# Kernel tuning notes

Hardware: AMD Instinct MI355X
Metric: run time of the kernel (lower is better)

Reference implementation:

```python
import jax, jax.numpy as jnp
import numpy as np


def setup_inputs() -> dict:
    key = jax.random.key(0)
    k1, k2, k3, k4 = jax.random.split(key, 4)
    b, h, w = 16, 28, 28
    C = 3072  # 1024 + 2048
    L1 = 9    # num_landmarks + 1
    K = 2000  # num_classes
    l3 = jax.random.normal(k1, (b, 1024, h, w), dtype=jnp.float32)
    l4 = jax.random.normal(k2, (b, 2048, h // 2, w // 2), dtype=jnp.float32)
    W_land = jax.random.normal(k3, (L1, C), dtype=jnp.float32) * 0.02  # 1x1 conv weight
    W_class = jax.random.normal(k4, (K, C), dtype=jnp.float32) * 0.02
    modulation = jnp.ones((1, C, L1), dtype=jnp.float32)
    return {"l3": l3, "l4": l4, "W_land": W_land, "W_class": W_class, "modulation": modulation}


def reference(l3, l4, W_land, W_class, modulation):
    b, c3, h, w = l3.shape
    # bilinear upsample layer4 to layer3 spatial size (align_corners=False semantics)
    l4_up = jax.image.resize(l4, (l4.shape[0], l4.shape[1], h, w), method="bilinear")
    x = jnp.concatenate([l4_up, l3], axis=1)  # (b, 3072, h, w)

    ab = jnp.einsum("lc,bchw->blhw", W_land, x)            # (b, L+1, h, w)
    b_sq = jnp.sum(x * x, axis=1, keepdims=True)           # (b, 1, h, w)
    a_sq = jnp.sum(W_land * W_land, axis=1)[None, :, None, None]  # (1, L+1, 1, 1)
    maps = jax.nn.softmax(-(b_sq - 2.0 * ab + a_sq), axis=1)      # channel softmax (Softmax2d)

    # weighted spatial pooling: mean over h and w of maps[:,None]*x[:,:,None]
    hw = h * w
    all_features = jnp.einsum("blhw,bchw->bcl", maps, x) / hw     # (b, C, L+1)

    # modulation; dropout layers are identity at inference
    modulated = all_features * modulation                           # (b, C, L+1)
    scores = jnp.einsum("kc,bcl->bkl", W_class, modulated)          # (b, K, L+1)
    class_scores = jnp.mean(scores[:, :, :-1], axis=-1)             # (b, K)
    return class_scores, maps, all_features
```

## Files before the change

### kernel.cpp

```cpp
#include <hip/hip_runtime.h>
#include <math.h>

#define C_TOTAL 3072
#define C4 2048
#define C3 1024
#define HW  784
#define W_  28
#define HW4 196
#define W4  14
#define L_TOT 9
#define NB  16
#define NK  2000
#define CH4 32
#define CH3 32
#define N3SUM (NB * L_TOT * HW)
#define N4SUM (NB * L_TOT * HW4)

__device__ __forceinline__ void up_taps(int o, int& i0, int& i1, float& w0, float& w1) {
    int j = o >> 1;
    if (o & 1) { i0 = j;                       i1 = (j + 1 < W4) ? j + 1 : W4 - 1; w0 = 0.75f; w1 = 0.25f; }
    else       { i0 = (j - 1 > 0) ? j - 1 : 0; i1 = j;                             w0 = 0.25f; w1 = 0.75f; }
}

__device__ __forceinline__ float wdown(int o, int s) {
    int i0, i1; float w0, w1;
    up_taps(o, i0, i1, w0, w1);
    return (i0 == s ? w0 : 0.f) + (i1 == s ? w1 : 0.f);
}

__global__ __launch_bounds__(256) void abx_kernel(
    const float* __restrict__ l3, const float* __restrict__ l4,
    const float* __restrict__ Wl,
    float* __restrict__ ab4p, float* __restrict__ ab3p, float* __restrict__ asqp)
{
    __shared__ float4 red[4][L_TOT][49];

    const int bx = blockIdx.x;
    const int b  = blockIdx.y;
    const int tid = threadIdx.x;

    if (bx < CH4) {
        const int s = tid >> 6;
        const int g = tid & 63;
        const int c0 = bx * 64;
        float4 acc[L_TOT];
        #pragma unroll
        for (int l = 0; l < L_TOT; ++l) acc[l] = make_float4(0.f, 0.f, 0.f, 0.f);
        if (g < 49) {
            const float4* slab = (const float4*)(l4 + ((size_t)b * C4 + c0) * HW4);
            #pragma unroll 8
            for (int i = 0; i < 16; ++i) {
                const int c = s * 16 + i;
                float4 xv = slab[c * 49 + g];
                const float* wc = Wl + c0 + c;
                #pragma unroll
                for (int l = 0; l < L_TOT; ++l) {
                    const float w = wc[l * C_TOTAL];
                    acc[l].x = fmaf(w, xv.x, acc[l].x);
                    acc[l].y = fmaf(w, xv.y, acc[l].y);
                    acc[l].z = fmaf(w, xv.z, acc[l].z);
                    acc[l].w = fmaf(w, xv.w, acc[l].w);
                }
            }
            #pragma unroll
            for (int l = 0; l < L_TOT; ++l) red[s][l][g] = acc[l];
        }
        __syncthreads();
        for (int v = tid; v < L_TOT * 49; v += 256) {
            const int l = v / 49, g2 = v % 49;
            float4 r0 = red[0][l][g2], r1 = red[1][l][g2];
            float4 r2 = red[2][l][g2], r3 = red[3][l][g2];
            float4 r = make_float4((r0.x + r1.x) + (r2.x + r3.x),
                                   (r0.y + r1.y) + (r2.y + r3.y),
                                   (r0.z + r1.z) + (r2.z + r3.z),
                                   (r0.w + r1.w) + (r2.w + r3.w));
            float4* out4 = (float4*)(ab4p + (size_t)(bx * NB + b) * (L_TOT * HW4));
            out4[v] = r;
        }
    } else if (bx < CH4 + CH3) {
        const int t = tid;
        const int j = bx - CH4;
        if (t >= HW / 4) return;
        const float4* l3b = (const float4*)(l3 + (size_t)b * C3 * HW);
        float4 acc[L_TOT];
        #pragma unroll
        for (int l = 0; l < L_TOT; ++l) acc[l] = make_float4(0.f, 0.f, 0.f, 0.f);
        const int c0 = j * (C3 / CH3);
        #pragma unroll 8
        for (int i = 0; i < C3 / CH3; ++i) {
            const int c = c0 + i;
            float4 xv = l3b[(size_t)c * (HW / 4) + t];
            const float* wc = Wl + C4 + c;
            #pragma unroll
            for (int l = 0; l < L_TOT; ++l) {
                const float w = wc[l * C_TOTAL];
                acc[l].x = fmaf(w, xv.x, acc[l].x);
                acc[l].y = fmaf(w, xv.y, acc[l].y);
                acc[l].z = fmaf(w, xv.z, acc[l].z);
                acc[l].w = fmaf(w, xv.w, acc[l].w);
            }
        }
        float4* outp = (float4*)(ab3p + (size_t)(j * NB + b) * (L_TOT * HW));
        #pragma unroll
        for (int l = 0; l < L_TOT; ++l) outp[l * (HW / 4) + t] = acc[l];
    } else {
        if (b != 0) return;
        __shared__ float redx[4];
        for (int l = 0; l < L_TOT; ++l) {
            const float* wrow = Wl + (size_t)l * C_TOTAL;
            float s0 = 0.f, s1 = 0.f, s2 = 0.f, s3 = 0.f;
            {
                float a = wrow[tid +  0 * 256];
                float bb = wrow[tid + 1 * 256];
                float c = wrow[tid +  2 * 256];
                float d = wrow[tid +  3 * 256];
                float e = wrow[tid +  4 * 256];
                float f = wrow[tid +  5 * 256];
                float gg = wrow[tid + 6 * 256];
                float h = wrow[tid +  7 * 256];
                float i2 = wrow[tid + 8 * 256];
                float j2 = wrow[tid + 9 * 256];
                float k2 = wrow[tid + 10 * 256];
                float m2 = wrow[tid + 11 * 256];
                s0 = fmaf(a, a, fmaf(e, e, i2 * i2));
                s1 = fmaf(bb, bb, fmaf(f, f, j2 * j2));
                s2 = fmaf(c, c, fmaf(gg, gg, k2 * k2));
                s3 = fmaf(d, d, fmaf(h, h, m2 * m2));
            }
            float s = (s0 + s1) + (s2 + s3);
            #pragma unroll
            for (int off = 32; off; off >>= 1) s += __shfl_down(s, off, 64);
            const int w = tid >> 6, lane = tid & 63;
            if (lane == 0) redx[w] = s;
            __syncthreads();
            if (tid == 0) asqp[l] = (redx[0] + redx[1]) + (redx[2] + redx[3]);
            __syncthreads();
        }
    }
}

__global__ __launch_bounds__(256) void reduce_kernel(
    const float* __restrict__ ab3p, const float* __restrict__ ab4p,
    float* __restrict__ absum, float* __restrict__ ab4sum)
{
    const int i4 = blockIdx.x * 256 + threadIdx.x;
    const int n3 = N3SUM / 4;
    if (i4 < n3) {
        const int b = i4 / (L_TOT * HW / 4), r = i4 - b * (L_TOT * HW / 4);
        const float4* src = (const float4*)ab3p;
        float4 s = make_float4(0.f, 0.f, 0.f, 0.f);
        #pragma unroll
        for (int j = 0; j < CH3; ++j) {
            float4 v = src[(size_t)(j * NB + b) * (L_TOT * HW / 4) + r];
            s.x += v.x; s.y += v.y; s.z += v.z; s.w += v.w;
        }
        ((float4*)absum)[i4] = s;
    } else {
        const int i2 = i4 - n3;
        if (i2 < N4SUM / 4) {
            const int b = i2 / (L_TOT * HW4 / 4), r = i2 - b * (L_TOT * HW4 / 4);
            const float4* src = (const float4*)ab4p;
            float4 s = make_float4(0.f, 0.f, 0.f, 0.f);
            #pragma unroll
            for (int j = 0; j < CH4; ++j) {
                float4 v = src[(size_t)(j * NB + b) * (L_TOT * HW4 / 4) + r];
                s.x += v.x; s.y += v.y; s.z += v.z; s.w += v.w;
            }
            ((float4*)ab4sum)[i2] = s;
        }
    }
}

__global__ __launch_bounds__(1024) void maps_fin_kernel(
    const float* __restrict__ absum, const float* __restrict__ ab4sum,
    const float* __restrict__ asqp, float* __restrict__ maps_out,
    float* __restrict__ mdown)
{
    __shared__ float msh[L_TOT * HW];
    __shared__ float ab4s[L_TOT * HW4];
    __shared__ float asq_s[L_TOT];

    const int tid = threadIdx.x;
    const int b   = blockIdx.x;

    for (int v = tid; v < L_TOT * HW4; v += 1024)
        ab4s[v] = ab4sum[(size_t)b * (L_TOT * HW4) + v];
    if (tid < L_TOT) asq_s[tid] = asqp[tid];
    __syncthreads();

    const int p = tid;
    if (p < HW) {
        const int y = p / W_, x = p % W_;
        int y0, y1, x0, x1; float wy0, wy1, wx0, wx1;
        up_taps(y, y0, y1, wy0, wy1);
        up_taps(x, x0, x1, wx0, wx1);

        const float* ap = absum + (size_t)b * (L_TOT * HW) + p;
        float lg[L_TOT];
        #pragma unroll
        for (int l = 0; l < L_TOT; ++l) {
            float s = ap[l * HW];
            const float* a = ab4s + l * HW4;
            float t0 = fmaf(a[y0 * W4 + x1], wx1, a[y0 * W4 + x0] * wx0);
            float t1 = fmaf(a[y1 * W4 + x1], wx1, a[y1 * W4 + x0] * wx0);
            float up = fmaf(t1, wy1, t0 * wy0);
            lg[l] = 2.f * (s + up) - asq_s[l];
        }
        float m = lg[0];
        #pragma unroll
        for (int l = 1; l < L_TOT; ++l) m = fmaxf(m, lg[l]);
        float sum = 0.f;
        #pragma unroll
        for (int l = 0; l < L_TOT; ++l) { lg[l] = __expf(lg[l] - m); sum += lg[l]; }
        const float inv = 1.f / sum;
        float* mp = maps_out + (size_t)b * L_TOT * HW + p;
        #pragma unroll
        for (int l = 0; l < L_TOT; ++l) {
            const float v = lg[l] * inv;
            mp[l * HW] = v;
            msh[l * HW + p] = v;
        }
    }
    __syncthreads();

    for (int v = tid; v < L_TOT * HW4; v += 1024) {
        const int l = v / HW4, q = v % HW4;
        const int sy = q / W4, sx = q % W4;
        float s = 0.f;
        int oy0 = 2 * sy - 1; if (oy0 < 0) oy0 = 0;
        int oy1 = 2 * sy + 2; if (oy1 > 27) oy1 = 27;
        int ox0 = 2 * sx - 1; if (ox0 < 0) ox0 = 0;
        int ox1 = 2 * sx + 2; if (ox1 > 27) ox1 = 27;
        for (int oy = oy0; oy <= oy1; ++oy) {
            const float wy = wdown(oy, sy);
            const float* row = msh + l * HW + oy * W_;
            for (int ox = ox0; ox <= ox1; ++ox)
                s = fmaf(wy * wdown(ox, sx), row[ox], s);
        }
        mdown[(size_t)b * (L_TOT * HW4) + v] = s;
    }
}

__global__ __launch_bounds__(256) void pool_kernel(
    const float* __restrict__ l3, const float* __restrict__ l4,
    const float* __restrict__ maps, const float* __restrict__ mdown,
    const float* __restrict__ modulation,
    float* __restrict__ af_out, float* __restrict__ g_out)
{
    __shared__ float msh[L_TOT * HW];

    const int tid  = threadIdx.x;
    const int b    = blockIdx.y;
    const int cblk = blockIdx.x;
    const bool isl4 = (cblk < 32);

    if (isl4) {
        const float4* src = (const float4*)(mdown + (size_t)b * (L_TOT * HW4));
        for (int v = tid; v < (L_TOT * HW4) / 4; v += 256)
            ((float4*)msh)[v] = src[v];
    } else {
        const float4* src = (const float4*)(maps + (size_t)b * L_TOT * HW);
        for (int v = tid; v < (L_TOT * HW) / 4; v += 256)
            ((float4*)msh)[v] = src[v];
    }
    __syncthreads();

    const int   PMAX  = isl4 ? HW4 : HW;
    const float* xbase = isl4 ? (l4 + (size_t)b * C4 * HW4)
                              : (l3 + (size_t)b * C3 * HW);
    const int cloc0 = (isl4 ? cblk : (cblk - 32)) * 64;
    const int w = tid >> 6, s = (tid >> 4) & 3, t = tid & 15;
    const int cl = cloc0 + w * 16 + s * 4;

    float acc[4][L_TOT];
    #pragma unroll
    for (int j = 0; j < 4; ++j)
        #pragma unroll
        for (int l = 0; l < L_TOT; ++l) acc[j][l] = 0.f;

    const int kmax = isl4 ? 4 : 13;
    for (int k = 0; k < kmax; ++k) {
        const int p = (t << 2) + (k << 6);
        if (p < PMAX) {
            float4 m4[L_TOT];
            #pragma unroll
            for (int l = 0; l < L_TOT; ++l) m4[l] = *(const float4*)&msh[l * PMAX + p];
            #pragma unroll
            for (int j = 0; j < 4; ++j) {
                float4 x4 = *(const float4*)&xbase[(size_t)(cl + j) * PMAX + p];
                #pragma unroll
                for (int l = 0; l < L_TOT; ++l)
                    acc[j][l] = fmaf(x4.x, m4[l].x, fmaf(x4.y, m4[l].y,
                                fmaf(x4.z, m4[l].z, fmaf(x4.w, m4[l].w, acc[j][l]))));
            }
        }
    }

    #pragma unroll
    for (int j = 0; j < 4; ++j)
        #pragma unroll
        for (int l = 0; l < L_TOT; ++l) {
            float v = acc[j][l];
            v += __shfl_xor(v, 1, 16);
            v += __shfl_xor(v, 2, 16);
            v += __shfl_xor(v, 4, 16);
            v += __shfl_xor(v, 8, 16);
            acc[j][l] = v;
        }

    if (t == 0) {
        const float inv_hw = 1.f / 784.f;
        #pragma unroll
        for (int j = 0; j < 4; ++j) {
            const int cg = (isl4 ? 0 : C4) + cl + j;
            float* afp = af_out + ((size_t)b * C_TOTAL + cg) * L_TOT;
            float gp = 0.f;
            #pragma unroll
            for (int l = 0; l < L_TOT; ++l) {
                float v = acc[j][l] * inv_hw;
                afp[l] = v;
                if (l < 8) gp = fmaf(modulation[cg * L_TOT + l], v, gp);
            }
            g_out[(size_t)b * C_TOTAL + cg] = gp * 0.125f;
        }
    }
}

__global__ __launch_bounds__(256) void class_kernel(
    const float* __restrict__ Wc, const float* __restrict__ g,
    float* __restrict__ out)
{
    const int wv   = threadIdx.x >> 6;
    const int lane = threadIdx.x & 63;
    const int k    = blockIdx.x * 4 + wv;

    const float4* w4p = (const float4*)(Wc + (size_t)k * C_TOTAL);
    float acc[NB];
    #pragma unroll
    for (int b = 0; b < NB; ++b) acc[b] = 0.f;

    for (int i = 0; i < C_TOTAL / 256; ++i) {
        const int c4i = i * 64 + lane;
        float4 w4 = w4p[c4i];
        #pragma unroll
        for (int b = 0; b < NB; ++b) {
            float4 g4 = ((const float4*)(g + (size_t)b * C_TOTAL))[c4i];
            acc[b] = fmaf(w4.x, g4.x, acc[b]);
            acc[b] = fmaf(w4.y, g4.y, acc[b]);
            acc[b] = fmaf(w4.z, g4.z, acc[b]);
            acc[b] = fmaf(w4.w, g4.w, acc[b]);
        }
    }
    #pragma unroll
    for (int b = 0; b < NB; ++b) {
        #pragma unroll
        for (int off = 32; off; off >>= 1) acc[b] += __shfl_down(acc[b], off, 64);
    }
    if (lane == 0) {
        #pragma unroll
        for (int b = 0; b < NB; ++b) out[(size_t)b * NK + k] = acc[b];
    }
}

extern "C" void kernel_launch(void* const* d_in, const int* in_sizes, int n_in,
                              void* d_out, int out_size, void* d_ws, size_t ws_size,
                              hipStream_t stream) {
    const float* l3  = (const float*)d_in[0];
    const float* l4  = (const float*)d_in[1];
    const float* Wl  = (const float*)d_in[2];
    const float* Wc  = (const float*)d_in[3];
    const float* mod = (const float*)d_in[4];

    float* out  = (float*)d_out;
    float* cls  = out;
    float* maps = out + 32000;
    float* af   = out + 144896;

    float* ab4p   = (float*)d_ws;
    float* ab3p   = ab4p + (size_t)CH4 * NB * L_TOT * HW4;
    float* absum  = ab3p + (size_t)CH3 * NB * L_TOT * HW;
    float* ab4sum = absum + N3SUM;
    float* asqp   = ab4sum + N4SUM;
    float* mdown  = asqp + 16;
    float* g      = mdown + N4SUM;

    abx_kernel     <<<dim3(CH4 + CH3 + 1, NB), 256, 0, stream>>>(l3, l4, Wl, ab4p, ab3p, asqp);
    reduce_kernel  <<<((N3SUM + N4SUM) / 4 + 255) / 256, 256, 0, stream>>>(ab3p, ab4p, absum, ab4sum);
    maps_fin_kernel<<<NB, 1024, 0, stream>>>(absum, ab4sum, asqp, maps, mdown);
    pool_kernel    <<<dim3(48, NB), 256, 0, stream>>>(l3, l4, maps, mdown, mod, af, g);
    class_kernel   <<<NK / 4, 256, 0, stream>>>(Wc, g, cls);
}
```

Baseline: 178.8 us.

## Fuse softmax map computation and downsampling into the pooling kernel

Removes the separate maps_fin kernel. Each pooling block now recomputes the softmax landmark maps for its batch from the reduced logits, keeps them in shared memory, and for layer4 blocks also computes the downsampled maps locally. One block per batch writes the maps output. This drops a launch and the global round trip of maps and mdown, at the cost of recomputing the softmax in every one of the 48 blocks per batch.

```diff
diff --git a/kernel.cpp b/kernel.cpp
--- a/kernel.cpp
+++ b/kernel.cpp
@@ -171,35 +171,37 @@
     }
 }
 
-__global__ __launch_bounds__(1024) void maps_fin_kernel(
+__global__ __launch_bounds__(256) void pool_kernel(
+    const float* __restrict__ l3, const float* __restrict__ l4,
     const float* __restrict__ absum, const float* __restrict__ ab4sum,
-    const float* __restrict__ asqp, float* __restrict__ maps_out,
-    float* __restrict__ mdown)
+    const float* __restrict__ asqp, const float* __restrict__ modulation,
+    float* __restrict__ maps_out, float* __restrict__ af_out, float* __restrict__ g_out)
 {
     __shared__ float msh[L_TOT * HW];
     __shared__ float ab4s[L_TOT * HW4];
+    __shared__ float mdsh[L_TOT * HW4];
     __shared__ float asq_s[L_TOT];
 
-    const int tid = threadIdx.x;
-    const int b   = blockIdx.x;
-
-    for (int v = tid; v < L_TOT * HW4; v += 1024)
+    const int tid  = threadIdx.x;
+    const int b    = blockIdx.y;
+    const int cblk = blockIdx.x;
+    const bool isl4 = (cblk < 32);
+
+    for (int v = tid; v < L_TOT * HW4; v += 256)
         ab4s[v] = ab4sum[(size_t)b * (L_TOT * HW4) + v];
     if (tid < L_TOT) asq_s[tid] = asqp[tid];
     __syncthreads();
 
-    const int p = tid;
-    if (p < HW) {
+    const float* ap = absum + (size_t)b * (L_TOT * HW);
+    for (int p = tid; p < HW; p += 256) {
         const int y = p / W_, x = p % W_;
         int y0, y1, x0, x1; float wy0, wy1, wx0, wx1;
         up_taps(y, y0, y1, wy0, wy1);
         up_taps(x, x0, x1, wx0, wx1);
-
-        const float* ap = absum + (size_t)b * (L_TOT * HW) + p;
         float lg[L_TOT];
         #pragma unroll
         for (int l = 0; l < L_TOT; ++l) {
-            float s = ap[l * HW];
+            float s = ap[l * HW + p];
             const float* a = ab4s + l * HW4;
             float t0 = fmaf(a[y0 * W4 + x1], wx1, a[y0 * W4 + x0] * wx0);
             float t1 = fmaf(a[y1 * W4 + x1], wx1, a[y1 * W4 + x0] * wx0);
@@ -213,59 +215,38 @@
         #pragma unroll
         for (int l = 0; l < L_TOT; ++l) { lg[l] = __expf(lg[l] - m); sum += lg[l]; }
         const float inv = 1.f / sum;
-        float* mp = maps_out + (size_t)b * L_TOT * HW + p;
-        #pragma unroll
-        for (int l = 0; l < L_TOT; ++l) {
-            const float v = lg[l] * inv;
-            mp[l * HW] = v;
-            msh[l * HW + p] = v;
-        }
+        #pragma unroll
+        for (int l = 0; l < L_TOT; ++l) msh[l * HW + p] = lg[l] * inv;
     }
     __syncthreads();
 
-    for (int v = tid; v < L_TOT * HW4; v += 1024) {
-        const int l = v / HW4, q = v % HW4;
-        const int sy = q / W4, sx = q % W4;
-        float s = 0.f;
-        int oy0 = 2 * sy - 1; if (oy0 < 0) oy0 = 0;
-        int oy1 = 2 * sy + 2; if (oy1 > 27) oy1 = 27;
-        int ox0 = 2 * sx - 1; if (ox0 < 0) ox0 = 0;
-        int ox1 = 2 * sx + 2; if (ox1 > 27) ox1 = 27;
-        for (int oy = oy0; oy <= oy1; ++oy) {
-            const float wy = wdown(oy, sy);
-            const float* row = msh + l * HW + oy * W_;
-            for (int ox = ox0; ox <= ox1; ++ox)
-                s = fmaf(wy * wdown(ox, sx), row[ox], s);
-        }
-        mdown[(size_t)b * (L_TOT * HW4) + v] = s;
-    }
-}
-
-__global__ __launch_bounds__(256) void pool_kernel(
-    const float* __restrict__ l3, const float* __restrict__ l4,
-    const float* __restrict__ maps, const float* __restrict__ mdown,
-    const float* __restrict__ modulation,
-    float* __restrict__ af_out, float* __restrict__ g_out)
-{
-    __shared__ float msh[L_TOT * HW];
-
-    const int tid  = threadIdx.x;
-    const int b    = blockIdx.y;
-    const int cblk = blockIdx.x;
-    const bool isl4 = (cblk < 32);
-
+    if (cblk == 32) {
+        float4* dst = (float4*)(maps_out + (size_t)b * L_TOT * HW);
+        const float4* src = (const float4*)msh;
+        for (int v = tid; v < (L_TOT * HW) / 4; v += 256) dst[v] = src[v];
+    }
     if (isl4) {
-        const float4* src = (const float4*)(mdown + (size_t)b * (L_TOT * HW4));
-        for (int v = tid; v < (L_TOT * HW4) / 4; v += 256)
-            ((float4*)msh)[v] = src[v];
-    } else {
-        const float4* src = (const float4*)(maps + (size_t)b * L_TOT * HW);
-        for (int v = tid; v < (L_TOT * HW) / 4; v += 256)
-            ((float4*)msh)[v] = src[v];
+        for (int v = tid; v < L_TOT * HW4; v += 256) {
+            const int l = v / HW4, q = v % HW4;
+            const int sy = q / W4, sx = q % W4;
+            float s = 0.f;
+            int oy0 = 2 * sy - 1; if (oy0 < 0) oy0 = 0;
+            int oy1 = 2 * sy + 2; if (oy1 > 27) oy1 = 27;
+            int ox0 = 2 * sx - 1; if (ox0 < 0) ox0 = 0;
+            int ox1 = 2 * sx + 2; if (ox1 > 27) ox1 = 27;
+            for (int oy = oy0; oy <= oy1; ++oy) {
+                const float wy = wdown(oy, sy);
+                const float* row = msh + l * HW + oy * W_;
+                for (int ox = ox0; ox <= ox1; ++ox)
+                    s = fmaf(wy * wdown(ox, sx), row[ox], s);
+            }
+            mdsh[v] = s;
+        }
     }
     __syncthreads();
 
     const int   PMAX  = isl4 ? HW4 : HW;
+    const float* mbase = isl4 ? mdsh : msh;
     const float* xbase = isl4 ? (l4 + (size_t)b * C4 * HW4)
                               : (l3 + (size_t)b * C3 * HW);
     const int cloc0 = (isl4 ? cblk : (cblk - 32)) * 64;
@@ -284,7 +265,7 @@
         if (p < PMAX) {
             float4 m4[L_TOT];
             #pragma unroll
-            for (int l = 0; l < L_TOT; ++l) m4[l] = *(const float4*)&msh[l * PMAX + p];
+            for (int l = 0; l < L_TOT; ++l) m4[l] = *(const float4*)&mbase[l * PMAX + p];
             #pragma unroll
             for (int j = 0; j < 4; ++j) {
                 float4 x4 = *(const float4*)&xbase[(size_t)(cl + j) * PMAX + p];
@@ -381,12 +362,10 @@
     float* absum  = ab3p + (size_t)CH3 * NB * L_TOT * HW;
     float* ab4sum = absum + N3SUM;
     float* asqp   = ab4sum + N4SUM;
-    float* mdown  = asqp + 16;
-    float* g      = mdown + N4SUM;
-
-    abx_kernel     <<<dim3(CH4 + CH3 + 1, NB), 256, 0, stream>>>(l3, l4, Wl, ab4p, ab3p, asqp);
-    reduce_kernel  <<<((N3SUM + N4SUM) / 4 + 255) / 256, 256, 0, stream>>>(ab3p, ab4p, absum, ab4sum);
-    maps_fin_kernel<<<NB, 1024, 0, stream>>>(absum, ab4sum, asqp, maps, mdown);
-    pool_kernel    <<<dim3(48, NB), 256, 0, stream>>>(l3, l4, maps, mdown, mod, af, g);
-    class_kernel   <<<NK / 4, 256, 0, stream>>>(Wc, g, cls);
-}
+    float* g      = asqp + 16;
+
+    abx_kernel   <<<dim3(CH4 + CH3 + 1, NB), 256, 0, stream>>>(l3, l4, Wl, ab4p, ab3p, asqp);
+    reduce_kernel<<<((N3SUM + N4SUM) / 4 + 255) / 256, 256, 0, stream>>>(ab3p, ab4p, absum, ab4sum);
+    pool_kernel  <<<dim3(48, NB), 256, 0, stream>>>(l3, l4, absum, ab4sum, asqp, mod, maps, af, g);
+    class_kernel <<<NK / 4, 256, 0, stream>>>(Wc, g, cls);
+}
```

Result: slower. 186.3 us (+4.2%).
